# Optimization experiments

Hardware: AMD Instinct MI355X
Metric: run time of the kernel (lower is better)

Reference implementation:

```python
import jax, jax.numpy as jnp
import numpy as np

D_MODEL = 1024
NHEAD = 16
D_K = D_MODEL // NHEAD
CHUNK = 256


def setup_inputs() -> dict:
    key = jax.random.key(0)
    ks = jax.random.split(key, 11)
    S, B = 4096, 4
    inp = {
        "query": jax.random.normal(ks[0], (S, B, D_MODEL), dtype=jnp.float32),
        "key": jax.random.normal(ks[1], (S, B, D_MODEL), dtype=jnp.float32),
        "value": jax.random.normal(ks[2], (S, B, D_MODEL), dtype=jnp.float32),
        # nn.Linear params: y = x @ W.T + b
        "Wq": jax.random.normal(ks[3], (D_MODEL, D_MODEL), dtype=jnp.float32) * 0.02,
        "bq": jnp.zeros((D_MODEL,), dtype=jnp.float32),
        "Wk": jax.random.normal(ks[4], (D_MODEL, D_MODEL), dtype=jnp.float32) * 0.02,
        "bk": jnp.zeros((D_MODEL,), dtype=jnp.float32),
        "Wv": jax.random.normal(ks[5], (D_MODEL, D_MODEL), dtype=jnp.float32) * 0.02,
        "bv": jnp.zeros((D_MODEL,), dtype=jnp.float32),
        "Wo": jax.random.normal(ks[6], (D_MODEL, D_MODEL), dtype=jnp.float32) * 0.02,
        "bo": jnp.zeros((D_MODEL,), dtype=jnp.float32),
    }
    return inp


def _split_heads(x, B):
    # (S, B, D) -> (B, H, S, d_k)
    S = x.shape[0]
    return x.reshape(S, B, NHEAD, D_K).transpose(1, 2, 0, 3)


def reference(query, key, value, Wq, bq, Wk, bk, Wv, bv, Wo, bo):
    S, B, _ = query.shape
    n_chunks = S // CHUNK  # S assumed divisible by CHUNK

    q = _split_heads(query @ Wq.T + bq, B)  # (B,H,S,dk)
    k = _split_heads(key @ Wk.T + bk, B)
    v = _split_heads(value @ Wv.T + bv, B)

    # Block-diagonal attention: softmax is strictly within each chunk.
    qc = q.reshape(B, NHEAD, n_chunks, CHUNK, D_K)
    kc = k.reshape(B, NHEAD, n_chunks, CHUNK, D_K)
    vc = v.reshape(B, NHEAD, n_chunks, CHUNK, D_K)

    scale = 1.0 / np.sqrt(D_K).astype(np.float32)
    scores = jnp.einsum("bhncd,bhnkd->bhnck", qc, kc) * scale  # (B,H,n,C,C)
    probs = jax.nn.softmax(scores, axis=-1)
    out = jnp.einsum("bhnck,bhnkd->bhncd", probs, vc)  # (B,H,n,C,dk)

    # (B,H,S,dk) -> (S,B,H*dk)
    out = out.reshape(B, NHEAD, S, D_K).transpose(2, 0, 1, 3).reshape(S, B, D_MODEL)
    return out @ Wo.T + bo
```

## Files before the change

kernel.cpp:

```cpp
#include <hip/hip_runtime.h>
#include <hip/hip_bf16.h>


namespace {

constexpr int kSeq = 4096, kB = 4, kDm = 1024, kNh = 16, kDk = 64, kChk = 256;
constexpr int kMr = kSeq * kB;
constexpr float kLog2e = 1.44269504088896340736f;

typedef __attribute__((ext_vector_type(8))) short bf16x8;
typedef __attribute__((ext_vector_type(4))) short bf16x4;
typedef __attribute__((ext_vector_type(4))) float f32x4;
typedef __attribute__((ext_vector_type(8))) unsigned short u16x8;
typedef __attribute__((ext_vector_type(4))) unsigned short u16x4;
typedef __attribute__((ext_vector_type(4))) unsigned u32x4;

#define AS1 __attribute__((address_space(1)))
#define AS3 __attribute__((address_space(3)))

__device__ __forceinline__ unsigned short f2bf(float x) {
  union { float f; unsigned u; } v; v.f = x;
  unsigned r = v.u + 0x7fffu + ((v.u >> 16) & 1u);
  return (unsigned short)(r >> 16);
}
__device__ __forceinline__ unsigned cvtpk(float lo, float hi) {
  unsigned r;
  asm("v_cvt_pk_bf16_f32 %0, %1, %2" : "=v"(r) : "v"(lo), "v"(hi));
  return r;
}
__device__ __forceinline__ int swz(int bo) { return bo ^ ((bo >> 3) & 0x70); }

__device__ __forceinline__ f32x4 mfma16x16(bf16x4 a, bf16x4 b, f32x4 c) {
#if __has_builtin(__builtin_amdgcn_mfma_f32_16x16x16bf16_1k)
  return __builtin_amdgcn_mfma_f32_16x16x16bf16_1k(a, b, c, 0, 0, 0);
#else
  asm volatile("v_mfma_f32_16x16x16_bf16 %0, %1, %2, %0\n\ts_nop 4"
               : "+v"(c) : "v"(a), "v"(b));
  return c;
#endif
}

__global__ __launch_bounds__(256) void cvt4(const float* __restrict__ s0,
                                            const float* __restrict__ s1,
                                            const float* __restrict__ s2,
                                            const float* __restrict__ s3,
                                            unsigned short* __restrict__ dst) {
  int i = blockIdx.x * 256 + threadIdx.x;
  int t = i >> 18;
  int j = i & 0x3ffff;
  const float* s = (t == 0) ? s0 : (t == 1) ? s1 : (t == 2) ? s2 : s3;
  f32x4 v = *(const f32x4*)(s + (size_t)j * 4);
  u16x4 o;
  o[0] = f2bf(v[0]); o[1] = f2bf(v[1]); o[2] = f2bf(v[2]); o[3] = f2bf(v[3]);
  *(u16x4*)(dst + (size_t)i * 4) = o;
}

__global__ __launch_bounds__(512, 2) void gemm_qkv8(
    const float* __restrict__ qf, const float* __restrict__ kf,
    const float* __restrict__ vf, const unsigned short* __restrict__ Wcat,
    const float* __restrict__ bq, const float* __restrict__ bk,
    const float* __restrict__ bv, unsigned short* __restrict__ dst, float sQ) {
  constexpr int K = kDm, nkt = K / 64;
  __shared__ unsigned short sh[65536];
  const int tid = (int)threadIdx.x;
  const int l = tid & 63;
  const int l15 = l & 15, l4 = l >> 4, l7 = l15 & 7;
  const int wid = tid >> 6, wm = wid >> 2, wn = wid & 3, wn1 = wn & 1;
  const int bid = (int)blockIdx.x;
  const int xcd = bid & 7, idx = bid >> 3;
  const int rbi = xcd * 8 + (idx & 7);
  const int cbi = idx >> 3;
  const int mat = cbi >> 2, ccol = (cbi & 3) * 256;
  const float* bp = (mat == 0) ? bq : (mat == 1) ? bk : bv;
  const float scale = (mat == 0) ? sQ : 1.0f;
  const float* Ain = (mat == 0) ? qf : (mat == 1) ? kf : vf;
  unsigned short* out = dst + (size_t)mat * kMr * kDm;

  const int arow = tid >> 2;
  const int ac2 = (tid & 3) * 2;
  const float* gA = Ain + (size_t)(rbi * 256 + arow) * K + ac2 * 8;
  const int awc0 = (ac2 ^ (arow & 7)) * 8;
  const int awc1 = ((ac2 + 1) ^ (arow & 7)) * 8;
  const int srow = tid >> 3;
  const int g16 = (tid & 7) ^ (srow & 7);
  const unsigned short* gB = Wcat + (size_t)(cbi * 256 + srow) * K + g16 * 8;
  const int ldsbase = (tid & ~63) * 8;

  auto stageB = [&](int T, int h) {
    const unsigned short* s = gB + (size_t)h * (128 * K) + T * 64;
    unsigned short* d = sh + 32768 + ((T & 1) * 2 + h) * 8192 + ldsbase;
    __builtin_amdgcn_global_load_lds((const AS1 unsigned int*)s, (AS3 unsigned int*)d, 16, 0, 0);
    __builtin_amdgcn_global_load_lds((const AS1 unsigned int*)(s + 64 * K),
                                     (AS3 unsigned int*)(d + 4096), 16, 0, 0);
  };
  auto loadA = [&](f32x4* r, int T, int h) {
    const float* s = gA + (size_t)h * (128 * K) + T * 64;
    r[0] = *(const f32x4*)s;
    r[1] = *(const f32x4*)(s + 4);
    r[2] = *(const f32x4*)(s + 8);
    r[3] = *(const f32x4*)(s + 12);
  };
  auto writeA = [&](const f32x4* r, int T, int h) {
    unsigned short* d = sh + ((T & 1) * 2 + h) * 8192 + arow * 64;
    u32x4 w0 = {cvtpk(r[0][0], r[0][1]), cvtpk(r[0][2], r[0][3]),
                cvtpk(r[1][0], r[1][1]), cvtpk(r[1][2], r[1][3])};
    u32x4 w1 = {cvtpk(r[2][0], r[2][1]), cvtpk(r[2][2], r[2][3]),
                cvtpk(r[3][0], r[3][1]), cvtpk(r[3][2], r[3][3])};
    *(u32x4*)(d + awc0) = w0;
    *(u32x4*)(d + awc1) = w1;
  };

  f32x4 acc[8][4] = {};
  f32x4 a0[2][4], a1[2][4];
  bf16x8 bfr[4];

  loadA(a0[0], 0, 0); loadA(a0[1], 0, 1);
  loadA(a1[0], 1, 0); loadA(a1[1], 1, 1);
  stageB(0, 0); stageB(0, 1);
  stageB(1, 0); stageB(1, 1);
  writeA(a0[0], 0, 0); writeA(a0[1], 0, 1);
  asm volatile("s_waitcnt lgkmcnt(0)" ::: "memory");
  asm volatile("s_waitcnt vmcnt(4)" ::: "memory");
  __builtin_amdgcn_s_barrier();

  for (int it = 0; it < nkt / 2; ++it) {
#pragma unroll
    for (int tt = 0; tt < 2; ++tt) {
      const int T = 2 * it + tt;
      const unsigned short* Asl = sh + (tt * 2 + wm) * 8192;
      const unsigned short* Bsl = sh + 32768 + (tt * 2 + (wn >> 1)) * 8192;
#pragma unroll
      for (int p = 0; p < 4; ++p) {
        const int kk = p >> 1, mfh = p & 1;
        bf16x8 af[4];
        const int sc = ((kk * 4 + l4) ^ l7) * 8;
        if (mfh == 0) {
#pragma unroll
          for (int nf = 0; nf < 4; ++nf)
            bfr[nf] = *(const bf16x8*)&Bsl[(wn1 * 64 + nf * 16 + l15) * 64 + sc];
        }
#pragma unroll
        for (int i = 0; i < 4; ++i)
          af[i] = *(const bf16x8*)&Asl[(mfh * 64 + i * 16 + l15) * 64 + sc];
        if (p == 0 && T + 2 < nkt) loadA(tt == 0 ? a0[0] : a1[0], T + 2, 0);
        if (p == 1 && T + 2 < nkt) loadA(tt == 0 ? a0[1] : a1[1], T + 2, 1);
        if (p == 3) {
          if (T + 2 < nkt) { stageB(T + 2, 0); stageB(T + 2, 1); }
          if (T + 1 < nkt) {
            writeA(tt == 0 ? a1[0] : a0[0], T + 1, 0);
            writeA(tt == 0 ? a1[1] : a0[1], T + 1, 1);
          }
        }
        __builtin_amdgcn_s_barrier();
        __builtin_amdgcn_s_setprio(1);
#pragma unroll
        for (int i = 0; i < 4; ++i)
#pragma unroll
          for (int nf = 0; nf < 4; ++nf)
            acc[mfh * 4 + i][nf] =
                __builtin_amdgcn_mfma_f32_16x16x32_bf16(af[i], bfr[nf], acc[mfh * 4 + i][nf], 0, 0, 0);
        __builtin_amdgcn_s_setprio(0);
        if (p == 3) {
          asm volatile("s_waitcnt lgkmcnt(0)" ::: "memory");
          if (T + 1 < nkt) {
            if (T + 2 < nkt) asm volatile("s_waitcnt vmcnt(12)" ::: "memory");
            else             asm volatile("s_waitcnt vmcnt(0)" ::: "memory");
          }
        }
        __builtin_amdgcn_s_barrier();
      }
    }
  }

#pragma unroll
  for (int mf = 0; mf < 8; ++mf)
#pragma unroll
    for (int nf = 0; nf < 4; ++nf) {
      int col = wn * 64 + nf * 16 + l15;
      float bvv = bp[ccol + col];
      int grpc = col >> 6;
      int c16 = (col & 63) >> 3, pos = col & 7;
      unsigned p01 = cvtpk((acc[mf][nf][0] + bvv) * scale, (acc[mf][nf][1] + bvv) * scale);
      unsigned p23 = cvtpk((acc[mf][nf][2] + bvv) * scale, (acc[mf][nf][3] + bvv) * scale);
      unsigned short ev[4] = {(unsigned short)p01, (unsigned short)(p01 >> 16),
                              (unsigned short)p23, (unsigned short)(p23 >> 16)};
#pragma unroll
      for (int j = 0; j < 4; ++j) {
        int tl = wm * 128 + mf * 16 + l4 * 4 + j;
        int grp = (tl & 3) * 4 + grpc;
        int u = (tl >> 2) * 8 + c16;
        int byte = (grp * 8192 + u * 16 + pos * 2) ^ (((u >> 3) & 7) << 4);
        *(unsigned short*)((char*)sh + byte) = ev[j];
      }
    }
  __syncthreads();
  {
    int inner = tid & 31, grp = tid >> 5;
    int b2 = grp >> 2, hl = grp & 3;
    int h = (cbi & 3) * 4 + hl;
    unsigned short* po = out + ((size_t)(b2 * kNh + h) * kSeq + rbi * 64) * kDk;
#pragma unroll
    for (int i = 0; i < 16; ++i) {
      int u = i * 32 + inner;
      int byte = (grp * 8192 + u * 16) ^ (((u >> 3) & 7) << 4);
      u16x8 v = *(const u16x8*)((const char*)sh + byte);
      *(u16x8*)(po + u * 8) = v;
    }
  }
}

__global__ __launch_bounds__(512, 2) void gemm_o8(const unsigned short* __restrict__ Aw,
                                                  const unsigned short* __restrict__ Bw,
                                                  const float* __restrict__ bias,
                                                  float* __restrict__ Cp) {
  constexpr int K = kDm, nkt = K / 64;
  __shared__ unsigned short sh[65536];
  const int tid = (int)threadIdx.x;
  const int l = tid & 63;
  const int l15 = l & 15, l4 = l >> 4, l7 = l15 & 7;
  const int wid = tid >> 6, wm = wid >> 2, wn = wid & 3, wn1 = wn & 1;
  const int bid = (int)blockIdx.x;
  const int xcd = bid & 7, idx = bid >> 3;
  const int rbi = xcd * 8 + (idx & 7);
  const int cbi = idx >> 3;
  const int rb = rbi * 256, cb = cbi * 256;

  const int srow = tid >> 3;
  const int g16 = (tid & 7) ^ (srow & 7);
  size_t abase[2][2];
#pragma unroll
  for (int h = 0; h < 2; ++h)
#pragma unroll
    for (int i = 0; i < 2; ++i) {
      int t = rb + h * 128 + srow + 64 * i;
      abase[h][i] = ((size_t)((t & 3) * kNh) * kSeq + (t >> 2)) * kDk + g16 * 8;
    }
  const unsigned short* gB = Bw + (size_t)(cb + srow) * K + g16 * 8;
  const int ldsbase = (tid & ~63) * 8;

  auto stageA = [&](int T, int h) {
    unsigned short* d = sh + ((T & 1) * 2 + h) * 8192 + ldsbase;
    size_t ko = (size_t)T * ((size_t)kSeq * kDk);
    __builtin_amdgcn_global_load_lds((const AS1 unsigned int*)(Aw + abase[h][0] + ko),
                                     (AS3 unsigned int*)d, 16, 0, 0);
    __builtin_amdgcn_global_load_lds((const AS1 unsigned int*)(Aw + abase[h][1] + ko),
                                     (AS3 unsigned int*)(d + 4096), 16, 0, 0);
  };
  auto stageB = [&](int T, int h) {
    const unsigned short* s = gB + (size_t)h * (128 * K) + T * 64;
    unsigned short* d = sh + 32768 + ((T & 1) * 2 + h) * 8192 + ldsbase;
    __builtin_amdgcn_global_load_lds((const AS1 unsigned int*)s, (AS3 unsigned int*)d, 16, 0, 0);
    __builtin_amdgcn_global_load_lds((const AS1 unsigned int*)(s + 64 * K),
                                     (AS3 unsigned int*)(d + 4096), 16, 0, 0);
  };

  f32x4 acc[8][4] = {};
  bf16x8 bfr[4];

  stageB(0, 0); stageB(0, 1);
  stageA(0, 0); stageA(0, 1);
  stageB(1, 0); stageB(1, 1);
  asm volatile("s_waitcnt vmcnt(4)" ::: "memory");
  __builtin_amdgcn_s_barrier();

  for (int it = 0; it < nkt / 2; ++it) {
#pragma unroll
    for (int tt = 0; tt < 2; ++tt) {
      const int T = 2 * it + tt;
      const unsigned short* Asl = sh + (tt * 2 + wm) * 8192;
      const unsigned short* Bsl = sh + 32768 + (tt * 2 + (wn >> 1)) * 8192;
#pragma unroll
      for (int p = 0; p < 4; ++p) {
        const int kk = p >> 1, mfh = p & 1;
        bf16x8 af[4];
        const int sc = ((kk * 4 + l4) ^ l7) * 8;
        if (mfh == 0) {
#pragma unroll
          for (int nf = 0; nf < 4; ++nf)
            bfr[nf] = *(const bf16x8*)&Bsl[(wn1 * 64 + nf * 16 + l15) * 64 + sc];
        }
#pragma unroll
        for (int i = 0; i < 4; ++i)
          af[i] = *(const bf16x8*)&Asl[(mfh * 64 + i * 16 + l15) * 64 + sc];
        if (p == 0 && T + 1 < nkt) stageA(T + 1, 0);
        if (p == 1 && T + 1 < nkt) stageA(T + 1, 1);
        if (p == 3 && T + 2 < nkt) { stageB(T + 2, 0); stageB(T + 2, 1); }
        __builtin_amdgcn_s_barrier();
        __builtin_amdgcn_s_setprio(1);
#pragma unroll
        for (int i = 0; i < 4; ++i)
#pragma unroll
          for (int nf = 0; nf < 4; ++nf)
            acc[mfh * 4 + i][nf] =
                __builtin_amdgcn_mfma_f32_16x16x32_bf16(af[i], bfr[nf], acc[mfh * 4 + i][nf], 0, 0, 0);
        __builtin_amdgcn_s_setprio(0);
        if (p == 3 && T + 1 < nkt) {
          if (T + 2 < nkt) asm volatile("s_waitcnt vmcnt(4)" ::: "memory");
          else             asm volatile("s_waitcnt vmcnt(0)" ::: "memory");
        }
        __builtin_amdgcn_s_barrier();
      }
    }
  }

#pragma unroll
  for (int nf = 0; nf < 4; ++nf) {
    int col = cb + wn * 64 + nf * 16 + l15;
    float bvv = bias[col];
#pragma unroll
    for (int mf = 0; mf < 8; ++mf) {
      int row0 = rb + wm * 128 + mf * 16 + l4 * 4;
#pragma unroll
      for (int j = 0; j < 4; ++j)
        Cp[(size_t)(row0 + j) * kDm + col] = acc[mf][nf][j] + bvv;
    }
  }
}

__global__ __launch_bounds__(256) void attn_blkdiag(const unsigned short* __restrict__ qw,
                                                    const unsigned short* __restrict__ kw,
                                                    const unsigned short* __restrict__ vw,
                                                    unsigned short* __restrict__ ow) {
  __shared__ unsigned short Kl[64 * 64];
  __shared__ unsigned short Vt[64 * 64];
  const int tid = (int)threadIdx.x;
  const int w = tid >> 6, l = tid & 63;
  const int l15 = l & 15, l4 = l >> 4;
  const int bid0 = (int)blockIdx.x;
  const int bid = (bid0 & 7) * 256 + (bid0 >> 3);
  const int hf = bid & 1, c = (bid >> 1) & 15, bh = bid >> 5;
  const size_t base = ((size_t)bh * kSeq + c * kChk) * kDk;
  const unsigned short* qp = qw + base + (size_t)hf * 128 * kDk;
  const unsigned short* kp = kw + base;
  const unsigned short* vp = vw + base;

  bf16x8 q[2][2];
#pragma unroll
  for (int m = 0; m < 2; ++m)
#pragma unroll
    for (int kk = 0; kk < 2; ++kk)
      q[m][kk] = *(const bf16x8*)(qp + (w * 32 + m * 16 + l15) * 64 + kk * 32 + l4 * 8);

  float mst[2] = {-1e30f, -1e30f}, lst[2] = {0.f, 0.f};
  f32x4 oacc[2][4] = {};

  const int r = tid >> 2, c0 = (tid & 3) * 16;
  u16x8 kr0, kr1, vr0, vr1;
  {
    const unsigned short* kt = kp + tid * 16;
    kr0 = *(const u16x8*)kt; kr1 = *(const u16x8*)(kt + 8);
    const unsigned short* vt = vp + tid * 16;
    vr0 = *(const u16x8*)vt; vr1 = *(const u16x8*)(vt + 8);
  }

  for (int kb = 0; kb < 4; ++kb) {
    __syncthreads();
    {
      int bo = r * 128 + c0 * 2;
      *(u16x8*)((char*)Kl + swz(bo)) = kr0;
      *(u16x8*)((char*)Kl + swz(bo + 16)) = kr1;
#pragma unroll
      for (int j = 0; j < 8; ++j) {
        *(unsigned short*)((char*)Vt + swz((c0 + j) * 128 + r * 2)) = vr0[j];
        *(unsigned short*)((char*)Vt + swz((c0 + 8 + j) * 128 + r * 2)) = vr1[j];
      }
    }
    __syncthreads();
    if (kb < 3) {
      const unsigned short* kt = kp + (kb + 1) * (64 * kDk) + tid * 16;
      kr0 = *(const u16x8*)kt; kr1 = *(const u16x8*)(kt + 8);
      const unsigned short* vt = vp + (kb + 1) * (64 * kDk) + tid * 16;
      vr0 = *(const u16x8*)vt; vr1 = *(const u16x8*)(vt + 8);
    }

    f32x4 sacc[4][2] = {};
    __builtin_amdgcn_s_setprio(1);
#pragma unroll
    for (int kk = 0; kk < 2; ++kk) {
      bf16x8 kf[4];
#pragma unroll
      for (int kn = 0; kn < 4; ++kn) {
        int bo = (kn * 16 + l15) * 128 + (kk * 32 + l4 * 8) * 2;
        kf[kn] = *(const bf16x8*)((const char*)Kl + swz(bo));
      }
#pragma unroll
      for (int kn = 0; kn < 4; ++kn)
#pragma unroll
        for (int m = 0; m < 2; ++m)
          sacc[kn][m] = __builtin_amdgcn_mfma_f32_16x16x32_bf16(kf[kn], q[m][kk], sacc[kn][m], 0, 0, 0);
    }
    __builtin_amdgcn_s_setprio(0);

    unsigned pw[2][4][2];
    float cbq[2][4];
#pragma unroll
    for (int m = 0; m < 2; ++m) {
      float rm = -1e30f;
#pragma unroll
      for (int kn = 0; kn < 4; ++kn)
#pragma unroll
        for (int j = 0; j < 4; ++j) rm = fmaxf(rm, sacc[kn][m][j]);
      rm = fmaxf(rm, __shfl_xor(rm, 16, 64));
      rm = fmaxf(rm, __shfl_xor(rm, 32, 64));
      float mn = fmaxf(mst[m], rm);
      float corr = exp2f(mst[m] - mn);
      mst[m] = mn;
      float rs = 0.f;
#pragma unroll
      for (int kn = 0; kn < 4; ++kn) {
#pragma unroll
        for (int j = 0; j < 4; ++j) {
          float p = exp2f(sacc[kn][m][j] - mn);
          sacc[kn][m][j] = p;
          rs += p;
        }
        pw[m][kn][0] = cvtpk(sacc[kn][m][0], sacc[kn][m][1]);
        pw[m][kn][1] = cvtpk(sacc[kn][m][2], sacc[kn][m][3]);
      }
      rs += __shfl_xor(rs, 16, 64);
      rs += __shfl_xor(rs, 32, 64);
      lst[m] = lst[m] * corr + rs;
#pragma unroll
      for (int j = 0; j < 4; ++j) cbq[m][j] = __shfl(corr, l4 * 4 + j, 64);
#pragma unroll
      for (int n = 0; n < 4; ++n)
#pragma unroll
        for (int j = 0; j < 4; ++j) oacc[m][n][j] *= cbq[m][j];
    }

    __builtin_amdgcn_s_setprio(1);
#pragma unroll
    for (int kn = 0; kn < 4; ++kn) {
      bf16x4 vf[4];
#pragma unroll
      for (int n = 0; n < 4; ++n) {
        int bo = (n * 16 + l15) * 128 + (kn * 16 + l4 * 4) * 2;
        vf[n] = *(const bf16x4*)((const char*)Vt + swz(bo));
      }
#pragma unroll
      for (int m = 0; m < 2; ++m) {
        union { unsigned u[2]; bf16x4 h; } pk;
        pk.u[0] = pw[m][kn][0]; pk.u[1] = pw[m][kn][1];
#pragma unroll
        for (int n = 0; n < 4; ++n)
          oacc[m][n] = mfma16x16(pk.h, vf[n], oacc[m][n]);
      }
    }
    __builtin_amdgcn_s_setprio(0);
  }

  unsigned short* op = ow + base + (size_t)hf * 128 * kDk;
#pragma unroll
  for (int m = 0; m < 2; ++m) {
    float inv = 1.f / lst[m];
#pragma unroll
    for (int j = 0; j < 4; ++j) {
      float ib = __shfl(inv, l4 * 4 + j, 64);
      int srow = w * 32 + m * 16 + l4 * 4 + j;
#pragma unroll
      for (int n = 0; n < 4; ++n)
        op[(size_t)srow * 64 + n * 16 + l15] = f2bf(oacc[m][n][j] * ib);
    }
  }
}

}

extern "C" void kernel_launch(void* const* d_in, const int* in_sizes, int n_in,
                              void* d_out, int out_size, void* d_ws, size_t ws_size,
                              hipStream_t stream) {
  const float* query = (const float*)d_in[0];
  const float* key   = (const float*)d_in[1];
  const float* value = (const float*)d_in[2];
  const float* Wq = (const float*)d_in[3];
  const float* bq = (const float*)d_in[4];
  const float* Wk = (const float*)d_in[5];
  const float* bk = (const float*)d_in[6];
  const float* Wv = (const float*)d_in[7];
  const float* bv = (const float*)d_in[8];
  const float* Wo = (const float*)d_in[9];
  const float* bo = (const float*)d_in[10];

  const float sQ = 0.125f * kLog2e;

  const size_t wsz = (size_t)kDm * kDm;
  const size_t tsz = (size_t)kMr * kDm;
  unsigned short* wsp = (unsigned short*)d_ws;
  unsigned short* wqb = wsp;
  unsigned short* wob = wqb + 3 * wsz;
  unsigned short* qws = wqb + 4 * wsz;
  unsigned short* kws = qws + tsz;
  unsigned short* vws = kws + tsz;
  unsigned short* aws = vws + tsz;

  const size_t need = (4 * wsz + 4 * tsz) * 2;
  if (ws_size < need) return;

  cvt4<<<dim3(4096), dim3(256), 0, stream>>>(Wq, Wk, Wv, Wo, wqb);
  gemm_qkv8<<<dim3(768), dim3(512), 0, stream>>>(query, key, value, wqb,
                                                 bq, bk, bv, qws, sQ);
  attn_blkdiag<<<dim3(2048), 256, 0, stream>>>(qws, kws, vws, aws);
  gemm_o8<<<dim3(256), dim3(512), 0, stream>>>(aws, wob, bo, (float*)d_out);
}
```

Before: 245.1 us.

## Convert QKV activations to bf16 once and reuse them across column blocks

The QKV GEMM is split into two launches. The first computes only the first column block of each projection and also writes the bf16-converted activations to workspace. The second computes the remaining column blocks and streams the bf16 activations straight into LDS with direct global-to-LDS loads, so fp32 activations are no longer re-read and re-converted per column block. This trades a smaller first launch that underfills the GPU, an extra kernel boundary and more workspace for less fp32 traffic and conversion work.

```diff
diff --git a/kernel.cpp b/kernel.cpp
--- a/kernel.cpp
+++ b/kernel.cpp
@@ -55,9 +55,11 @@
   *(u16x4*)(dst + (size_t)i * 4) = o;
 }
 
+template <int MODE>
 __global__ __launch_bounds__(512, 2) void gemm_qkv8(
     const float* __restrict__ qf, const float* __restrict__ kf,
-    const float* __restrict__ vf, const unsigned short* __restrict__ Wcat,
+    const float* __restrict__ vf, unsigned short* __restrict__ abf,
+    const unsigned short* __restrict__ Wcat,
     const float* __restrict__ bq, const float* __restrict__ bk,
     const float* __restrict__ bv, unsigned short* __restrict__ dst, float sQ) {
   constexpr int K = kDm, nkt = K / 64;
@@ -68,13 +70,24 @@
   const int wid = tid >> 6, wm = wid >> 2, wn = wid & 3, wn1 = wn & 1;
   const int bid = (int)blockIdx.x;
   const int xcd = bid & 7, idx = bid >> 3;
-  const int rbi = xcd * 8 + (idx & 7);
-  const int cbi = idx >> 3;
+  int rbi, cbi;
+  if constexpr (MODE == 0) {
+    rbi = xcd * 8 + (idx & 7);
+    int c9 = idx >> 3;
+    cbi = (c9 / 3) * 4 + 1 + (c9 % 3);
+  } else if constexpr (MODE == 1) {
+    rbi = xcd * 8 + (idx & 7);
+    cbi = (idx >> 3) * 4;
+  } else {
+    rbi = xcd * 8 + (idx & 7);
+    cbi = idx >> 3;
+  }
   const int mat = cbi >> 2, ccol = (cbi & 3) * 256;
   const float* bp = (mat == 0) ? bq : (mat == 1) ? bk : bv;
   const float scale = (mat == 0) ? sQ : 1.0f;
   const float* Ain = (mat == 0) ? qf : (mat == 1) ? kf : vf;
   unsigned short* out = dst + (size_t)mat * kMr * kDm;
+  unsigned short* abfm = abf + (size_t)mat * kMr * kDm;
 
   const int arow = tid >> 2;
   const int ac2 = (tid & 3) * 2;
@@ -84,11 +97,19 @@
   const int srow = tid >> 3;
   const int g16 = (tid & 7) ^ (srow & 7);
   const unsigned short* gB = Wcat + (size_t)(cbi * 256 + srow) * K + g16 * 8;
+  const unsigned short* gAb = abfm + (size_t)(rbi * 256 + srow) * K + g16 * 8;
   const int ldsbase = (tid & ~63) * 8;
 
   auto stageB = [&](int T, int h) {
     const unsigned short* s = gB + (size_t)h * (128 * K) + T * 64;
     unsigned short* d = sh + 32768 + ((T & 1) * 2 + h) * 8192 + ldsbase;
+    __builtin_amdgcn_global_load_lds((const AS1 unsigned int*)s, (AS3 unsigned int*)d, 16, 0, 0);
+    __builtin_amdgcn_global_load_lds((const AS1 unsigned int*)(s + 64 * K),
+                                     (AS3 unsigned int*)(d + 4096), 16, 0, 0);
+  };
+  auto stageAb = [&](int T, int h) {
+    const unsigned short* s = gAb + (size_t)h * (128 * K) + T * 64;
+    unsigned short* d = sh + ((T & 1) * 2 + h) * 8192 + ldsbase;
     __builtin_amdgcn_global_load_lds((const AS1 unsigned int*)s, (AS3 unsigned int*)d, 16, 0, 0);
     __builtin_amdgcn_global_load_lds((const AS1 unsigned int*)(s + 64 * K),
                                      (AS3 unsigned int*)(d + 4096), 16, 0, 0);
@@ -108,19 +129,35 @@
                 cvtpk(r[3][0], r[3][1]), cvtpk(r[3][2], r[3][3])};
     *(u32x4*)(d + awc0) = w0;
     *(u32x4*)(d + awc1) = w1;
+    if constexpr (MODE == 1) {
+      unsigned short* g =
+          abfm + (size_t)(rbi * 256 + h * 128 + arow) * K + T * 64 + ac2 * 8;
+      *(u32x4*)g = w0;
+      *(u32x4*)(g + 8) = w1;
+    }
   };
 
   f32x4 acc[8][4] = {};
   f32x4 a0[2][4], a1[2][4];
   bf16x8 bfr[4];
 
-  loadA(a0[0], 0, 0); loadA(a0[1], 0, 1);
-  loadA(a1[0], 1, 0); loadA(a1[1], 1, 1);
-  stageB(0, 0); stageB(0, 1);
-  stageB(1, 0); stageB(1, 1);
-  writeA(a0[0], 0, 0); writeA(a0[1], 0, 1);
-  asm volatile("s_waitcnt lgkmcnt(0)" ::: "memory");
-  asm volatile("s_waitcnt vmcnt(4)" ::: "memory");
+  if constexpr (MODE == 0) {
+    stageB(0, 0); stageB(0, 1);
+    stageAb(0, 0); stageAb(0, 1);
+    stageB(1, 0); stageB(1, 1);
+    asm volatile("s_waitcnt vmcnt(4)" ::: "memory");
+  } else {
+    loadA(a0[0], 0, 0); loadA(a0[1], 0, 1);
+    loadA(a1[0], 1, 0); loadA(a1[1], 1, 1);
+    stageB(0, 0); stageB(0, 1);
+    stageB(1, 0); stageB(1, 1);
+    writeA(a0[0], 0, 0); writeA(a0[1], 0, 1);
+    asm volatile("s_waitcnt lgkmcnt(0)" ::: "memory");
+    if constexpr (MODE == 1)
+      asm volatile("s_waitcnt vmcnt(8)" ::: "memory");
+    else
+      asm volatile("s_waitcnt vmcnt(4)" ::: "memory");
+  }
   __builtin_amdgcn_s_barrier();
 
   for (int it = 0; it < nkt / 2; ++it) {
@@ -142,13 +179,19 @@
 #pragma unroll
         for (int i = 0; i < 4; ++i)
           af[i] = *(const bf16x8*)&Asl[(mfh * 64 + i * 16 + l15) * 64 + sc];
-        if (p == 0 && T + 2 < nkt) loadA(tt == 0 ? a0[0] : a1[0], T + 2, 0);
-        if (p == 1 && T + 2 < nkt) loadA(tt == 0 ? a0[1] : a1[1], T + 2, 1);
-        if (p == 3) {
-          if (T + 2 < nkt) { stageB(T + 2, 0); stageB(T + 2, 1); }
-          if (T + 1 < nkt) {
-            writeA(tt == 0 ? a1[0] : a0[0], T + 1, 0);
-            writeA(tt == 0 ? a1[1] : a0[1], T + 1, 1);
+        if constexpr (MODE == 0) {
+          if (p == 0 && T + 1 < nkt) stageAb(T + 1, 0);
+          if (p == 1 && T + 1 < nkt) stageAb(T + 1, 1);
+          if (p == 3 && T + 2 < nkt) { stageB(T + 2, 0); stageB(T + 2, 1); }
+        } else {
+          if (p == 0 && T + 2 < nkt) loadA(tt == 0 ? a0[0] : a1[0], T + 2, 0);
+          if (p == 1 && T + 2 < nkt) loadA(tt == 0 ? a0[1] : a1[1], T + 2, 1);
+          if (p == 3) {
+            if (T + 2 < nkt) { stageB(T + 2, 0); stageB(T + 2, 1); }
+            if (T + 1 < nkt) {
+              writeA(tt == 0 ? a1[0] : a0[0], T + 1, 0);
+              writeA(tt == 0 ? a1[1] : a0[1], T + 1, 1);
+            }
           }
         }
         __builtin_amdgcn_s_barrier();
@@ -161,10 +204,22 @@
                 __builtin_amdgcn_mfma_f32_16x16x32_bf16(af[i], bfr[nf], acc[mfh * 4 + i][nf], 0, 0, 0);
         __builtin_amdgcn_s_setprio(0);
         if (p == 3) {
-          asm volatile("s_waitcnt lgkmcnt(0)" ::: "memory");
-          if (T + 1 < nkt) {
-            if (T + 2 < nkt) asm volatile("s_waitcnt vmcnt(12)" ::: "memory");
-            else             asm volatile("s_waitcnt vmcnt(0)" ::: "memory");
+          if constexpr (MODE == 0) {
+            if (T + 1 < nkt) {
+              if (T + 2 < nkt) asm volatile("s_waitcnt vmcnt(4)" ::: "memory");
+              else             asm volatile("s_waitcnt vmcnt(0)" ::: "memory");
+            }
+          } else {
+            asm volatile("s_waitcnt lgkmcnt(0)" ::: "memory");
+            if (T + 1 < nkt) {
+              if constexpr (MODE == 1) {
+                if (T + 2 < nkt) asm volatile("s_waitcnt vmcnt(16)" ::: "memory");
+                else             asm volatile("s_waitcnt vmcnt(4)" ::: "memory");
+              } else {
+                if (T + 2 < nkt) asm volatile("s_waitcnt vmcnt(12)" ::: "memory");
+                else             asm volatile("s_waitcnt vmcnt(0)" ::: "memory");
+              }
+            }
           }
         }
         __builtin_amdgcn_s_barrier();
@@ -491,14 +546,28 @@
   unsigned short* qws = wqb + 4 * wsz;
   unsigned short* kws = qws + tsz;
   unsigned short* vws = kws + tsz;
-  unsigned short* aws = vws + tsz;
-
-  const size_t need = (4 * wsz + 4 * tsz) * 2;
-  if (ws_size < need) return;
+  unsigned short* x0  = vws + tsz;
+
+  const size_t needA = (4 * wsz + 6 * tsz) * 2;
+  const size_t needB = (4 * wsz + 4 * tsz) * 2;
+  if (ws_size < needB) return;
 
   cvt4<<<dim3(4096), dim3(256), 0, stream>>>(Wq, Wk, Wv, Wo, wqb);
-  gemm_qkv8<<<dim3(768), dim3(512), 0, stream>>>(query, key, value, wqb,
-                                                 bq, bk, bv, qws, sQ);
-  attn_blkdiag<<<dim3(2048), 256, 0, stream>>>(qws, kws, vws, aws);
-  gemm_o8<<<dim3(256), dim3(512), 0, stream>>>(aws, wob, bo, (float*)d_out);
-}
+
+  if (ws_size >= needA) {
+    unsigned short* abf = x0;
+    unsigned short* aws = abf;
+    gemm_qkv8<1><<<dim3(192), dim3(512), 0, stream>>>(query, key, value, abf, wqb,
+                                                      bq, bk, bv, qws, sQ);
+    gemm_qkv8<0><<<dim3(576), dim3(512), 0, stream>>>(query, key, value, abf, wqb,
+                                                      bq, bk, bv, qws, sQ);
+    attn_blkdiag<<<dim3(2048), 256, 0, stream>>>(qws, kws, vws, aws);
+    gemm_o8<<<dim3(256), dim3(512), 0, stream>>>(aws, wob, bo, (float*)d_out);
+  } else {
+    unsigned short* aws = x0;
+    gemm_qkv8<2><<<dim3(768), dim3(512), 0, stream>>>(query, key, value, aws ,
+                                                      wqb, bq, bk, bv, qws, sQ);
+    attn_blkdiag<<<dim3(2048), 256, 0, stream>>>(qws, kws, vws, aws);
+    gemm_o8<<<dim3(256), dim3(512), 0, stream>>>(aws, wob, bo, (float*)d_out);
+  }
+}
```

Result: slower. 286.1 us (+16.7%).

## Split QKV GEMM tile across sixteen waves with single-tile A prefetch

Applied to the files above, without the earlier changes.

The fused QKV projection GEMM now runs 1024 threads per block instead of 512. Each wave computes a 64x64 sub-tile instead of 128x64, and the A/B staging loads and the epilogue store loop are re-partitioned over the larger thread count. The fp32 A prefetch distance drops from two K-tiles to one, which halves the per-thread A staging registers. The aim is more waves in flight to hide latency, at the cost of less register-level reuse per wave. The launch bound also requests 4 blocks per CU, which may force heavy register limits or spills given the 128KB of LDS per block.

```diff
diff --git a/kernel.cpp b/kernel.cpp
--- a/kernel.cpp
+++ b/kernel.cpp
@@ -55,7 +55,7 @@
   *(u16x4*)(dst + (size_t)i * 4) = o;
 }
 
-__global__ __launch_bounds__(512, 2) void gemm_qkv8(
+__global__ __launch_bounds__(1024, 4) void gemm_qkv8(
     const float* __restrict__ qf, const float* __restrict__ kf,
     const float* __restrict__ vf, const unsigned short* __restrict__ Wcat,
     const float* __restrict__ bq, const float* __restrict__ bk,
@@ -65,7 +65,8 @@
   const int tid = (int)threadIdx.x;
   const int l = tid & 63;
   const int l15 = l & 15, l4 = l >> 4, l7 = l15 & 7;
-  const int wid = tid >> 6, wm = wid >> 2, wn = wid & 3, wn1 = wn & 1;
+  const int wid = tid >> 6;
+  const int wm = wid >> 2, wn = wid & 3;
   const int bid = (int)blockIdx.x;
   const int xcd = bid & 7, idx = bid >> 3;
   const int rbi = xcd * 8 + (idx & 7);
@@ -76,11 +77,9 @@
   const float* Ain = (mat == 0) ? qf : (mat == 1) ? kf : vf;
   unsigned short* out = dst + (size_t)mat * kMr * kDm;
 
-  const int arow = tid >> 2;
-  const int ac2 = (tid & 3) * 2;
-  const float* gA = Ain + (size_t)(rbi * 256 + arow) * K + ac2 * 8;
-  const int awc0 = (ac2 ^ (arow & 7)) * 8;
-  const int awc1 = ((ac2 + 1) ^ (arow & 7)) * 8;
+  const int ar = tid >> 3, ac = tid & 7;
+  const float* gA = Ain + (size_t)(rbi * 256 + ar) * K + ac * 8;
+  const int awp = (ac ^ (ar & 7)) * 8;
   const int srow = tid >> 3;
   const int g16 = (tid & 7) ^ (srow & 7);
   const unsigned short* gB = Wcat + (size_t)(cbi * 256 + srow) * K + g16 * 8;
@@ -90,82 +89,74 @@
     const unsigned short* s = gB + (size_t)h * (128 * K) + T * 64;
     unsigned short* d = sh + 32768 + ((T & 1) * 2 + h) * 8192 + ldsbase;
     __builtin_amdgcn_global_load_lds((const AS1 unsigned int*)s, (AS3 unsigned int*)d, 16, 0, 0);
-    __builtin_amdgcn_global_load_lds((const AS1 unsigned int*)(s + 64 * K),
-                                     (AS3 unsigned int*)(d + 4096), 16, 0, 0);
   };
   auto loadA = [&](f32x4* r, int T, int h) {
     const float* s = gA + (size_t)h * (128 * K) + T * 64;
     r[0] = *(const f32x4*)s;
     r[1] = *(const f32x4*)(s + 4);
-    r[2] = *(const f32x4*)(s + 8);
-    r[3] = *(const f32x4*)(s + 12);
   };
   auto writeA = [&](const f32x4* r, int T, int h) {
-    unsigned short* d = sh + ((T & 1) * 2 + h) * 8192 + arow * 64;
-    u32x4 w0 = {cvtpk(r[0][0], r[0][1]), cvtpk(r[0][2], r[0][3]),
-                cvtpk(r[1][0], r[1][1]), cvtpk(r[1][2], r[1][3])};
-    u32x4 w1 = {cvtpk(r[2][0], r[2][1]), cvtpk(r[2][2], r[2][3]),
-                cvtpk(r[3][0], r[3][1]), cvtpk(r[3][2], r[3][3])};
-    *(u32x4*)(d + awc0) = w0;
-    *(u32x4*)(d + awc1) = w1;
+    unsigned short* d = sh + ((T & 1) * 2 + h) * 8192 + ar * 64;
+    u32x4 w = {cvtpk(r[0][0], r[0][1]), cvtpk(r[0][2], r[0][3]),
+               cvtpk(r[1][0], r[1][1]), cvtpk(r[1][2], r[1][3])};
+    *(u32x4*)(d + awp) = w;
   };
 
-  f32x4 acc[8][4] = {};
-  f32x4 a0[2][4], a1[2][4];
+  f32x4 acc[4][4] = {};
+  f32x4 a0[2], a1[2];
   bf16x8 bfr[4];
 
-  loadA(a0[0], 0, 0); loadA(a0[1], 0, 1);
-  loadA(a1[0], 1, 0); loadA(a1[1], 1, 1);
+  loadA(a0, 0, 0); loadA(a1, 0, 1);
   stageB(0, 0); stageB(0, 1);
   stageB(1, 0); stageB(1, 1);
-  writeA(a0[0], 0, 0); writeA(a0[1], 0, 1);
+  writeA(a0, 0, 0); writeA(a1, 0, 1);
   asm volatile("s_waitcnt lgkmcnt(0)" ::: "memory");
-  asm volatile("s_waitcnt vmcnt(4)" ::: "memory");
+  asm volatile("s_waitcnt vmcnt(2)" ::: "memory");
   __builtin_amdgcn_s_barrier();
 
   for (int it = 0; it < nkt / 2; ++it) {
 #pragma unroll
     for (int tt = 0; tt < 2; ++tt) {
       const int T = 2 * it + tt;
-      const unsigned short* Asl = sh + (tt * 2 + wm) * 8192;
+      const unsigned short* Asl = sh + (tt * 2 + (wm >> 1)) * 8192;
       const unsigned short* Bsl = sh + 32768 + (tt * 2 + (wn >> 1)) * 8192;
+      const int arow0 = (wm & 1) * 64;
+      const int brow0 = (wn & 1) * 64;
 #pragma unroll
       for (int p = 0; p < 4; ++p) {
         const int kk = p >> 1, mfh = p & 1;
-        bf16x8 af[4];
+        bf16x8 af[2];
         const int sc = ((kk * 4 + l4) ^ l7) * 8;
         if (mfh == 0) {
 #pragma unroll
           for (int nf = 0; nf < 4; ++nf)
-            bfr[nf] = *(const bf16x8*)&Bsl[(wn1 * 64 + nf * 16 + l15) * 64 + sc];
-        }
-#pragma unroll
-        for (int i = 0; i < 4; ++i)
-          af[i] = *(const bf16x8*)&Asl[(mfh * 64 + i * 16 + l15) * 64 + sc];
-        if (p == 0 && T + 2 < nkt) loadA(tt == 0 ? a0[0] : a1[0], T + 2, 0);
-        if (p == 1 && T + 2 < nkt) loadA(tt == 0 ? a0[1] : a1[1], T + 2, 1);
+            bfr[nf] = *(const bf16x8*)&Bsl[(brow0 + nf * 16 + l15) * 64 + sc];
+        }
+#pragma unroll
+        for (int i = 0; i < 2; ++i)
+          af[i] = *(const bf16x8*)&Asl[(arow0 + mfh * 32 + i * 16 + l15) * 64 + sc];
+        if (p == 0 && T + 1 < nkt) loadA(a0, T + 1, 0);
+        if (p == 1 && T + 1 < nkt) loadA(a1, T + 1, 1);
         if (p == 3) {
           if (T + 2 < nkt) { stageB(T + 2, 0); stageB(T + 2, 1); }
           if (T + 1 < nkt) {
-            writeA(tt == 0 ? a1[0] : a0[0], T + 1, 0);
-            writeA(tt == 0 ? a1[1] : a0[1], T + 1, 1);
+            writeA(a0, T + 1, 0);
+            writeA(a1, T + 1, 1);
           }
         }
         __builtin_amdgcn_s_barrier();
         __builtin_amdgcn_s_setprio(1);
 #pragma unroll
-        for (int i = 0; i < 4; ++i)
+        for (int i = 0; i < 2; ++i)
 #pragma unroll
           for (int nf = 0; nf < 4; ++nf)
-            acc[mfh * 4 + i][nf] =
-                __builtin_amdgcn_mfma_f32_16x16x32_bf16(af[i], bfr[nf], acc[mfh * 4 + i][nf], 0, 0, 0);
+            acc[mfh * 2 + i][nf] =
+                __builtin_amdgcn_mfma_f32_16x16x32_bf16(af[i], bfr[nf], acc[mfh * 2 + i][nf], 0, 0, 0);
         __builtin_amdgcn_s_setprio(0);
         if (p == 3) {
           asm volatile("s_waitcnt lgkmcnt(0)" ::: "memory");
-          if (T + 1 < nkt) {
-            if (T + 2 < nkt) asm volatile("s_waitcnt vmcnt(12)" ::: "memory");
-            else             asm volatile("s_waitcnt vmcnt(0)" ::: "memory");
-          }
+          if (T + 1 == nkt - 1)
+            asm volatile("s_waitcnt vmcnt(0)" ::: "memory");
         }
         __builtin_amdgcn_s_barrier();
       }
@@ -173,7 +164,7 @@
   }
 
 #pragma unroll
-  for (int mf = 0; mf < 8; ++mf)
+  for (int mf = 0; mf < 4; ++mf)
 #pragma unroll
     for (int nf = 0; nf < 4; ++nf) {
       int col = wn * 64 + nf * 16 + l15;
@@ -186,7 +177,7 @@
                               (unsigned short)p23, (unsigned short)(p23 >> 16)};
 #pragma unroll
       for (int j = 0; j < 4; ++j) {
-        int tl = wm * 128 + mf * 16 + l4 * 4 + j;
+        int tl = wm * 64 + mf * 16 + l4 * 4 + j;
         int grp = (tl & 3) * 4 + grpc;
         int u = (tl >> 2) * 8 + c16;
         int byte = (grp * 8192 + u * 16 + pos * 2) ^ (((u >> 3) & 7) << 4);
@@ -195,13 +186,13 @@
     }
   __syncthreads();
   {
-    int inner = tid & 31, grp = tid >> 5;
+    int inner = tid & 63, grp = tid >> 6;
     int b2 = grp >> 2, hl = grp & 3;
     int h = (cbi & 3) * 4 + hl;
     unsigned short* po = out + ((size_t)(b2 * kNh + h) * kSeq + rbi * 64) * kDk;
 #pragma unroll
-    for (int i = 0; i < 16; ++i) {
-      int u = i * 32 + inner;
+    for (int i = 0; i < 8; ++i) {
+      int u = i * 64 + inner;
       int byte = (grp * 8192 + u * 16) ^ (((u >> 3) & 7) << 4);
       u16x8 v = *(const u16x8*)((const char*)sh + byte);
       *(u16x8*)(po + u * 8) = v;
@@ -497,8 +488,8 @@
   if (ws_size < need) return;
 
   cvt4<<<dim3(4096), dim3(256), 0, stream>>>(Wq, Wk, Wv, Wo, wqb);
-  gemm_qkv8<<<dim3(768), dim3(512), 0, stream>>>(query, key, value, wqb,
-                                                 bq, bk, bv, qws, sQ);
+  gemm_qkv8<<<dim3(768), dim3(1024), 0, stream>>>(query, key, value, wqb,
+                                                  bq, bk, bv, qws, sQ);
   attn_blkdiag<<<dim3(2048), 256, 0, stream>>>(qws, kws, vws, aws);
   gemm_o8<<<dim3(256), dim3(512), 0, stream>>>(aws, wob, bo, (float*)d_out);
 }
```

Result: no change. 242.1 us (median of 3 runs) (-1.2%).
